# Kernel tuning notes

Hardware: AMD Instinct MI355X
Metric: run time of the kernel (lower is better)

## Reference

```python
import jax, jax.numpy as jnp
import numpy as np

THRESHOLD = 0.1
LN_EPS = 1e-5


def _ternary(w):
    # sign(w), zeroed where |w| < threshold (BitNet-style ternary quantization)
    return jnp.where(jnp.abs(w) < THRESHOLD, 0.0, jnp.sign(w))


def _layernorm(x, gamma, beta):
    mu = jnp.mean(x, axis=-1, keepdims=True)
    var = jnp.var(x, axis=-1, keepdims=True)
    return (x - mu) * jax.lax.rsqrt(var + LN_EPS) * gamma + beta


def setup_inputs() -> dict:
    key = jax.random.key(0)
    ks = jax.random.split(key, 3)
    N, D_IN, D_H, D_OUT = 8192, 2048, 8192, 2048
    x = jax.random.normal(ks[0], (N, D_IN), dtype=jnp.float32)
    # Weights uniform in (-0.2, 0.2) so the 0.1 ternary threshold yields a
    # nontrivial mix of {-1, 0, +1} (torch init uses (-0.1, 0.1) which would
    # quantize to all zeros; same math, more informative test values).
    w1 = jax.random.uniform(ks[1], (D_H, D_IN), minval=-0.2, maxval=0.2, dtype=jnp.float32)
    w2 = jax.random.uniform(ks[2], (D_OUT, D_H), minval=-0.2, maxval=0.2, dtype=jnp.float32)
    return {
        "x": x,
        "w1": w1, "b1": jnp.zeros((D_H,), jnp.float32), "s1": jnp.ones((D_H,), jnp.float32),
        "w2": w2, "b2": jnp.zeros((D_OUT,), jnp.float32), "s2": jnp.ones((D_OUT,), jnp.float32),
        "ln1_g": jnp.ones((D_H,), jnp.float32), "ln1_b": jnp.zeros((D_H,), jnp.float32),
        "out_g": jnp.ones((D_OUT,), jnp.float32), "out_b": jnp.zeros((D_OUT,), jnp.float32),
    }


def reference(x, w1, b1, s1, w2, b2, s2, ln1_g, ln1_b, out_g, out_b):
    # layer 1: ternary linear + learned per-output scale
    h = (jnp.einsum('nd,hd->nh', x, _ternary(w1)) + b1) * s1
    h = jax.nn.relu(_layernorm(h, ln1_g, ln1_b))
    # layer 2
    o = (jnp.einsum('nh,oh->no', h, _ternary(w2)) + b2) * s2
    return _layernorm(o, out_g, out_b)
```

## Files before the change

### kernel.cpp

```cpp
#include <hip/hip_runtime.h>


#define THRESH 0.1f
#define LN_EPS 1e-5f

typedef _Float16 f16x8 __attribute__((ext_vector_type(8)));
typedef float f32x4 __attribute__((ext_vector_type(4)));

typedef __attribute__((address_space(3))) void lds_void;
typedef const __attribute__((address_space(1))) void glob_void;

__device__ __forceinline__ void gld16(const void* g, void* l) {
  __builtin_amdgcn_global_load_lds((glob_void*)g, (lds_void*)l, 16, 0, 0);
}


__global__ __launch_bounds__(256) void cvt_x_f16(const float* __restrict__ x,
                                                 _Float16* __restrict__ y) {
  const long i = ((long)blockIdx.x * 256 + threadIdx.x) * 8;
  const float4 v0 = *(const float4*)(x + i);
  const float4 v1 = *(const float4*)(x + i + 4);
  const float a[8] = {v0.x, v0.y, v0.z, v0.w, v1.x, v1.y, v1.z, v1.w};
  f16x8 o;
#pragma unroll
  for (int e = 0; e < 8; ++e) o[e] = (_Float16)a[e];
  *(f16x8*)(y + i) = o;
}

__global__ __launch_bounds__(256) void quant_w(const float* __restrict__ w,
                                               _Float16* __restrict__ t) {
  const long i = ((long)blockIdx.x * 256 + threadIdx.x) * 8;
  const float4 v0 = *(const float4*)(w + i);
  const float4 v1 = *(const float4*)(w + i + 4);
  const float a[8] = {v0.x, v0.y, v0.z, v0.w, v1.x, v1.y, v1.z, v1.w};
  f16x8 o;
#pragma unroll
  for (int e = 0; e < 8; ++e) {
    const float q = (fabsf(a[e]) < THRESH) ? 0.f : (a[e] > 0.f ? 1.f : -1.f);
    o[e] = (_Float16)q;
  }
  *(f16x8*)(t + i) = o;
}


#define BARF()                       \
  __builtin_amdgcn_s_barrier();      \
  asm volatile("" ::: "memory")
#define LGKM0() asm volatile("s_waitcnt lgkmcnt(0)" ::: "memory")
#define VMC4() asm volatile("s_waitcnt vmcnt(4)" ::: "memory")
#define VMC0() asm volatile("s_waitcnt vmcnt(0)" ::: "memory")

#define MFMA_QUAD(m0)                                                                        \
  __builtin_amdgcn_s_setprio(1);                                                             \
  _Pragma("unroll") for (int i = 0; i < 4; ++i)                                              \
  _Pragma("unroll") for (int j = 0; j < 4; ++j)                                              \
      acc[(m0) + i][j] = __builtin_amdgcn_mfma_f32_16x16x32_f16(af[i], bf[j],                \
                                                                acc[(m0) + i][j], 0, 0, 0); \
  __builtin_amdgcn_s_setprio(0)

template <bool OUT_F16>
__global__ __launch_bounds__(512, 2) void gemm256(const _Float16* __restrict__ A,
                                                  const _Float16* __restrict__ B,
                                                  void* __restrict__ C,
                                                  const float* __restrict__ bias,
                                                  const float* __restrict__ scale,
                                                  int N, int K) {
  __shared__ _Float16 sA[2][2][8192];
  __shared__ _Float16 sB[2][2][8192];

  const int tid = threadIdx.x;
  const int lane = tid & 63;
  const int wave = tid >> 6;
  const int wm = wave >> 2;
  const int wn = wave & 3;
  const long row0 = (long)blockIdx.y * 256;
  const long col0 = (long)blockIdx.x * 256;

  const int c0 = tid, c1 = tid + 512;
  const _Float16* pA0 = A + (row0 + ((c0 >> 6) << 4) + (c0 & 15)) * (long)K + (((c0 >> 4) & 3) << 3);
  const _Float16* pA1 = A + (row0 + ((c1 >> 6) << 4) + (c1 & 15)) * (long)K + (((c1 >> 4) & 3) << 3);
  const _Float16* pB0 = B + (col0 + ((c0 >> 6) << 4) + (c0 & 15)) * (long)K + (((c0 >> 4) & 3) << 3);
  const _Float16* pB1 = B + (col0 + ((c1 >> 6) << 4) + (c1 & 15)) * (long)K + (((c1 >> 4) & 3) << 3);

#define STG_A(nx, kh, koff)                     \
  gld16(pA0 + (koff), &sA[nx][kh][c0 * 8]);     \
  gld16(pA1 + (koff), &sA[nx][kh][c1 * 8])
#define STG_B(nx, kh, koff)                     \
  gld16(pB0 + (koff), &sB[nx][kh][c0 * 8]);     \
  gld16(pB1 + (koff), &sB[nx][kh][c1 * 8])

  f32x4 acc[8][4] = {};
  const int nT = K >> 6;
  const int aoff = wm * 8 * 512 + lane * 8;
  const int boff = wn * 4 * 512 + lane * 8;

  STG_A(0, 0, 0);
  STG_B(0, 0, 0);
  STG_A(0, 1, 32);
  STG_B(0, 1, 32);
  VMC4();
  BARF();

  for (int t = 0; t < nT; ++t) {
    const int cur = t & 1, nx = cur ^ 1;
    const bool more = (t + 1 < nT);
    const int kn = (t + 1) << 6;

    f16x8 af[4], bf[4];

#pragma unroll
    for (int i = 0; i < 4; ++i) af[i] = *(const f16x8*)&sA[cur][0][aoff + i * 512];
#pragma unroll
    for (int j = 0; j < 4; ++j) bf[j] = *(const f16x8*)&sB[cur][0][boff + j * 512];
    if (more) { STG_A(nx, 0, kn); }
    BARF();
    LGKM0();
    MFMA_QUAD(0);
    BARF();

#pragma unroll
    for (int i = 0; i < 4; ++i) af[i] = *(const f16x8*)&sA[cur][0][aoff + (4 + i) * 512];
    if (more) {
      STG_B(nx, 0, kn);
      VMC4();
    } else {
      VMC0();
    }
    BARF();
    LGKM0();
    MFMA_QUAD(4);
    BARF();

#pragma unroll
    for (int i = 0; i < 4; ++i) af[i] = *(const f16x8*)&sA[cur][1][aoff + i * 512];
#pragma unroll
    for (int j = 0; j < 4; ++j) bf[j] = *(const f16x8*)&sB[cur][1][boff + j * 512];
    if (more) { STG_A(nx, 1, kn + 32); }
    BARF();
    LGKM0();
    MFMA_QUAD(0);
    BARF();

#pragma unroll
    for (int i = 0; i < 4; ++i) af[i] = *(const f16x8*)&sA[cur][1][aoff + (4 + i) * 512];
    if (more) {
      STG_B(nx, 1, kn + 32);
      VMC4();
    }
    BARF();
    LGKM0();
    MFMA_QUAD(4);
    BARF();
  }

  const int qd = lane >> 4, l16 = lane & 15;
#pragma unroll
  for (int nf = 0; nf < 4; ++nf) {
    const long c = col0 + wn * 64 + nf * 16 + l16;
    const float bb = bias[c];
    const float ss = scale[c];
#pragma unroll
    for (int mf = 0; mf < 8; ++mf) {
      const long r = row0 + wm * 128 + mf * 16 + qd * 4;
#pragma unroll
      for (int reg = 0; reg < 4; ++reg) {
        const float v = (acc[mf][nf][reg] + bb) * ss;
        if constexpr (OUT_F16)
          ((_Float16*)C)[(r + reg) * (long)N + c] = (_Float16)v;
        else
          ((float*)C)[(r + reg) * (long)N + c] = v;
      }
    }
  }
}


__global__ __launch_bounds__(256) void ln_relu_rows_f16(_Float16* __restrict__ h,
                                                        const float* __restrict__ g,
                                                        const float* __restrict__ b) {
  const int D = 8192;
  const long base = (long)blockIdx.x * D;
  const int tid = threadIdx.x;
  f16x8 v[4];
  float sum = 0.f, sq = 0.f;
#pragma unroll
  for (int c = 0; c < 4; ++c) {
    v[c] = *(const f16x8*)&h[base + c * 2048 + tid * 8];
#pragma unroll
    for (int e = 0; e < 8; ++e) {
      const float f = (float)v[c][e];
      sum += f;
      sq += f * f;
    }
  }
#pragma unroll
  for (int off = 32; off > 0; off >>= 1) {
    sum += __shfl_down(sum, off);
    sq += __shfl_down(sq, off);
  }
  __shared__ float rs[4], rq[4];
  const int wv = tid >> 6, ln = tid & 63;
  if (ln == 0) { rs[wv] = sum; rq[wv] = sq; }
  __syncthreads();
  sum = rs[0] + rs[1] + rs[2] + rs[3];
  sq = rq[0] + rq[1] + rq[2] + rq[3];
  const float mu = sum / D;
  const float rstd = rsqrtf(sq / D - mu * mu + LN_EPS);
#pragma unroll
  for (int c = 0; c < 4; ++c) {
    const int col = c * 2048 + tid * 8;
    f16x8 o;
#pragma unroll
    for (int e = 0; e < 8; ++e) {
      const float f = ((float)v[c][e] - mu) * rstd * g[col + e] + b[col + e];
      o[e] = (_Float16)fmaxf(f, 0.f);
    }
    *(f16x8*)&h[base + col] = o;
  }
}

__global__ __launch_bounds__(256) void ln_rows_f32_inplace(float* __restrict__ io,
                                                           const float* __restrict__ g,
                                                           const float* __restrict__ b) {
  const int D = 2048;
  const long base = (long)blockIdx.x * D;
  const int tid = threadIdx.x;
  const float4 v0 = *(const float4*)&io[base + tid * 8];
  const float4 v1 = *(const float4*)&io[base + tid * 8 + 4];
  const float a[8] = {v0.x, v0.y, v0.z, v0.w, v1.x, v1.y, v1.z, v1.w};
  float sum = 0.f, sq = 0.f;
#pragma unroll
  for (int e = 0; e < 8; ++e) {
    sum += a[e];
    sq += a[e] * a[e];
  }
#pragma unroll
  for (int off = 32; off > 0; off >>= 1) {
    sum += __shfl_down(sum, off);
    sq += __shfl_down(sq, off);
  }
  __shared__ float rs[4], rq[4];
  const int wv = tid >> 6, ln = tid & 63;
  if (ln == 0) { rs[wv] = sum; rq[wv] = sq; }
  __syncthreads();
  sum = rs[0] + rs[1] + rs[2] + rs[3];
  sq = rq[0] + rq[1] + rq[2] + rq[3];
  const float mu = sum / D;
  const float rstd = rsqrtf(sq / D - mu * mu + LN_EPS);
  const int col = tid * 8;
  float o[8];
#pragma unroll
  for (int e = 0; e < 8; ++e) o[e] = (a[e] - mu) * rstd * g[col + e] + b[col + e];
  *(float4*)&io[base + col] = make_float4(o[0], o[1], o[2], o[3]);
  *(float4*)&io[base + col + 4] = make_float4(o[4], o[5], o[6], o[7]);
}


extern "C" void kernel_launch(void* const* d_in, const int* in_sizes, int n_in,
                              void* d_out, int out_size, void* d_ws, size_t ws_size,
                              hipStream_t stream) {
  const float* x    = (const float*)d_in[0];
  const float* w1   = (const float*)d_in[1];
  const float* b1   = (const float*)d_in[2];
  const float* s1   = (const float*)d_in[3];
  const float* w2   = (const float*)d_in[4];
  const float* b2   = (const float*)d_in[5];
  const float* s2   = (const float*)d_in[6];
  const float* ln1g = (const float*)d_in[7];
  const float* ln1b = (const float*)d_in[8];
  const float* outg = (const float*)d_in[9];
  const float* outb = (const float*)d_in[10];

  const int N = 8192, D_IN = 2048, D_H = 8192, D_OUT = 2048;
  const size_t MB = 1024 * 1024;
  char* ob = (char*)d_out;
  _Float16* xh  = (_Float16*)(ob);
  _Float16* tw1 = (_Float16*)(ob + 32 * MB);
  char* ws = (char*)d_ws;
  _Float16* tw2 = (_Float16*)(ws);
  _Float16* h   = (_Float16*)(ws + 32 * MB);

  cvt_x_f16<<<(N * D_IN) / 2048, 256, 0, stream>>>(x, xh);
  quant_w<<<(D_H * D_IN) / 2048, 256, 0, stream>>>(w1, tw1);
  quant_w<<<(D_OUT * D_H) / 2048, 256, 0, stream>>>(w2, tw2);

  gemm256<true><<<dim3(D_H / 256, N / 256), 512, 0, stream>>>(xh, tw1, h, b1, s1, D_H, D_IN);
  ln_relu_rows_f16<<<N, 256, 0, stream>>>(h, ln1g, ln1b);

  gemm256<false><<<dim3(D_OUT / 256, N / 256), 512, 0, stream>>>(h, tw2, d_out, b2, s2, D_OUT, D_H);
  ln_rows_f32_inplace<<<N, 256, 0, stream>>>((float*)d_out, outg, outb);
}
```

Baseline: 902.1 us.

## Deepen GEMM prefetch pipeline and preload both A fragment halves per phase

Restructures the double-buffered GEMM main loop so global-to-LDS loads run one half-tile further ahead. The next-next K half-tile is written into the current buffer's first half as soon as that half has been consumed, with waits relaxed to vmcnt(8). Each phase now reads both A fragment sets up front, and the explicit lgkmcnt(0) waits are dropped in favour of compiler-inserted ones. The aim is to hide global load latency and reduce barrier-bound stalls between MFMA groups, at the cost of more live registers and more outstanding loads.

```diff
diff --git a/kernel.cpp b/kernel.cpp
--- a/kernel.cpp
+++ b/kernel.cpp
@@ -46,15 +46,15 @@
 #define BARF()                       \
   __builtin_amdgcn_s_barrier();      \
   asm volatile("" ::: "memory")
-#define LGKM0() asm volatile("s_waitcnt lgkmcnt(0)" ::: "memory")
+#define VMC8() asm volatile("s_waitcnt vmcnt(8)" ::: "memory")
 #define VMC4() asm volatile("s_waitcnt vmcnt(4)" ::: "memory")
 #define VMC0() asm volatile("s_waitcnt vmcnt(0)" ::: "memory")
 
-#define MFMA_QUAD(m0)                                                                        \
+#define MFMA_QUAD(m0, AF)                                                                    \
   __builtin_amdgcn_s_setprio(1);                                                             \
   _Pragma("unroll") for (int i = 0; i < 4; ++i)                                              \
   _Pragma("unroll") for (int j = 0; j < 4; ++j)                                              \
-      acc[(m0) + i][j] = __builtin_amdgcn_mfma_f32_16x16x32_f16(af[i], bf[j],                \
+      acc[(m0) + i][j] = __builtin_amdgcn_mfma_f32_16x16x32_f16(AF[i], bf[j],                \
                                                                 acc[(m0) + i][j], 0, 0, 0); \
   __builtin_amdgcn_s_setprio(0)
 
@@ -98,58 +98,63 @@
   STG_B(0, 0, 0);
   STG_A(0, 1, 32);
   STG_B(0, 1, 32);
-  VMC4();
+  if (nT > 1) {
+    STG_A(1, 0, 64);
+    STG_B(1, 0, 64);
+    VMC8();
+  } else {
+    VMC4();
+  }
   BARF();
 
   for (int t = 0; t < nT; ++t) {
     const int cur = t & 1, nx = cur ^ 1;
-    const bool more = (t + 1 < nT);
-    const int kn = (t + 1) << 6;
-
-    f16x8 af[4], bf[4];
+    const bool more1 = (t + 1 < nT);
+    const bool more2 = (t + 2 < nT);
+    const int kn1 = (t + 1) << 6;
+    const int kn2 = (t + 2) << 6;
+
+    f16x8 af[4], af2[4], bf[4];
 
 #pragma unroll
     for (int i = 0; i < 4; ++i) af[i] = *(const f16x8*)&sA[cur][0][aoff + i * 512];
 #pragma unroll
     for (int j = 0; j < 4; ++j) bf[j] = *(const f16x8*)&sB[cur][0][boff + j * 512];
-    if (more) { STG_A(nx, 0, kn); }
-    BARF();
-    LGKM0();
-    MFMA_QUAD(0);
-    BARF();
-
-#pragma unroll
-    for (int i = 0; i < 4; ++i) af[i] = *(const f16x8*)&sA[cur][0][aoff + (4 + i) * 512];
-    if (more) {
-      STG_B(nx, 0, kn);
-      VMC4();
+#pragma unroll
+    for (int i = 0; i < 4; ++i) af2[i] = *(const f16x8*)&sA[cur][0][aoff + (4 + i) * 512];
+    if (more1) { STG_A(nx, 1, kn1 + 32); }
+    BARF();
+    MFMA_QUAD(0, af);
+    BARF();
+
+    if (more1) {
+      STG_B(nx, 1, kn1 + 32);
+      VMC8();
     } else {
       VMC0();
     }
     BARF();
-    LGKM0();
-    MFMA_QUAD(4);
+    MFMA_QUAD(4, af2);
     BARF();
 
 #pragma unroll
     for (int i = 0; i < 4; ++i) af[i] = *(const f16x8*)&sA[cur][1][aoff + i * 512];
 #pragma unroll
     for (int j = 0; j < 4; ++j) bf[j] = *(const f16x8*)&sB[cur][1][boff + j * 512];
-    if (more) { STG_A(nx, 1, kn + 32); }
-    BARF();
-    LGKM0();
-    MFMA_QUAD(0);
-    BARF();
-
-#pragma unroll
-    for (int i = 0; i < 4; ++i) af[i] = *(const f16x8*)&sA[cur][1][aoff + (4 + i) * 512];
-    if (more) {
-      STG_B(nx, 1, kn + 32);
-      VMC4();
-    }
-    BARF();
-    LGKM0();
-    MFMA_QUAD(4);
+#pragma unroll
+    for (int i = 0; i < 4; ++i) af2[i] = *(const f16x8*)&sA[cur][1][aoff + (4 + i) * 512];
+    if (more2) { STG_A(cur, 0, kn2); }
+    BARF();
+    MFMA_QUAD(0, af);
+    BARF();
+
+    if (more2) { STG_B(cur, 0, kn2); }
+    if (more1) {
+      if (more2) VMC8();
+      else       VMC4();
+    }
+    BARF();
+    MFMA_QUAD(4, af2);
     BARF();
   }
 
```

Measured after the change: 968.3 us. 7.3% more time.
